# Optimization experiments

Hardware: AMD Instinct MI355X
Metric: run time of the kernel (lower is better)

The kernel has to match this reference:

```python
import jax, jax.numpy as jnp
import numpy as np

H = 16
LN_EPS = 1e-5


def setup_inputs() -> dict:
    key = jax.random.key(0)
    ks = jax.random.split(key, 8)
    B, N, D = 2, 2048, 1024
    s = D ** -0.5
    return {
        "q_s": jax.random.normal(ks[0], (B, N, D), jnp.float32),
        "pos_emb": jax.random.normal(ks[1], (B, N, D), jnp.float32),
        "Wq": jax.random.normal(ks[2], (D, D), jnp.float32) * s,
        "Wk": jax.random.normal(ks[3], (D, D), jnp.float32) * s,
        "Wv": jax.random.normal(ks[4], (D, D), jnp.float32) * s,
        "Wo": jax.random.normal(ks[5], (D, D), jnp.float32) * s,
        "bo": jnp.zeros((D,), jnp.float32),
        "ln_g": jnp.ones((D,), jnp.float32),
        "ln_b": jnp.zeros((D,), jnp.float32),
    }


def _split_heads(t):
    b, n, d = t.shape
    return t.reshape(b, n, H, d // H).transpose(0, 2, 1, 3)  # b h n d


def reference(q_s, pos_emb, Wq, Wk, Wv, Wo, bo, ln_g, ln_b):
    # self-attention: k_s = v_s = q_s
    q = _split_heads(q_s @ Wq)
    k = _split_heads(q_s @ Wk)
    v = _split_heads(q_s @ Wv)
    p = _split_heads(pos_emb)
    scale = q.shape[-1] ** -0.5
    # content-content + content-position attention logits: [b,h,i,j]
    att = (jnp.einsum('bhid,bhjd->bhij', q, k) + jnp.einsum('bhid,bhjd->bhij', q, p)) * scale
    att = jax.nn.softmax(att, axis=-1)
    o = jnp.einsum('bhij,bhjd->bhid', att, v)
    b, h, n, d = o.shape
    o = o.transpose(0, 2, 1, 3).reshape(b, n, h * d)
    o = o @ Wo + bo  # out_layer (dropout rate 0 -> identity)
    x = o + q_s  # residual
    mu = jnp.mean(x, axis=-1, keepdims=True)
    var = jnp.var(x, axis=-1, keepdims=True)
    return (x - mu) * jax.lax.rsqrt(var + LN_EPS) * ln_g + ln_b
```

## Files before the change

### kernel.cpp

```cpp
#include <hip/hip_runtime.h>
#include <hip/hip_bf16.h>
#include <stdint.h>

typedef unsigned short u16;
typedef unsigned int u32;
typedef short s16x8 __attribute__((ext_vector_type(8)));
typedef short s16x4 __attribute__((ext_vector_type(4)));
typedef float f32x4 __attribute__((ext_vector_type(4)));

#define MFMA(a, b, c) __builtin_amdgcn_mfma_f32_16x16x32_bf16((a), (b), (c), 0, 0, 0)

__device__ __forceinline__ u16 f2bf_rte(float f) {
  __hip_bfloat16 h = __float2bfloat16(f);
  u16 u;
  __builtin_memcpy(&u, &h, 2);
  return u;
}

__device__ __forceinline__ void gload16(const u16* g, u16* l) {
  __builtin_amdgcn_global_load_lds((const __attribute__((address_space(1))) u32*)g,
                                   (__attribute__((address_space(3))) u32*)l, 16, 0, 0);
}

__global__ __launch_bounds__(256) void k_cvt(const float* __restrict__ in,
                                             u16* __restrict__ out, int n8) {
  int i = blockIdx.x * 256 + threadIdx.x;
  if (i >= n8) return;
  const f32x4* p = (const f32x4*)(in + (size_t)i * 8);
  f32x4 a = p[0], b = p[1];
  s16x8 o;
  for (int k = 0; k < 4; ++k) o[k] = (short)f2bf_rte(a[k]);
  for (int k = 0; k < 4; ++k) o[4 + k] = (short)f2bf_rte(b[k]);
  *(s16x8*)(out + (size_t)i * 8) = o;
}

__global__ __launch_bounds__(256) void k_transpose_w(const float* __restrict__ W0,
                                                     const float* __restrict__ W1,
                                                     const float* __restrict__ W2,
                                                     const float* __restrict__ W3,
                                                     u16* __restrict__ out) {
  const int z = blockIdx.z;
  const float* in = (z == 0) ? W0 : (z == 1) ? W1 : (z == 2) ? W2 : W3;
  u16* o = out + (size_t)z * 1024 * 1024;
  __shared__ u16 tile[64][65];
  const int t = threadIdx.x, tx = t & 63, ty = t >> 6;
  const int r0 = blockIdx.y * 64, c0 = blockIdx.x * 64;
  for (int rr = 0; rr < 16; ++rr) {
    int row = rr * 4 + ty;
    tile[row][tx] = f2bf_rte(in[(size_t)(r0 + row) * 1024 + c0 + tx]);
  }
  __syncthreads();
  for (int rr = 0; rr < 16; ++rr) {
    int row = rr * 4 + ty;
    o[(size_t)(c0 + row) * 1024 + r0 + tx] = tile[tx][row];
  }
}

__global__ __launch_bounds__(256) void k_transpose_v(const u16* __restrict__ V,
                                                     u16* __restrict__ Vt) {
  __shared__ u16 tile[64][65];
  const int t = threadIdx.x, tx = t & 63, ty = t >> 6;
  const int j0 = blockIdx.x * 64;
  const int bh = blockIdx.y;
  const u16* src = V + (size_t)bh * 2048 * 64;
  u16* dst = Vt + (size_t)bh * 64 * 2048;
  for (int rr = 0; rr < 16; ++rr) {
    int row = rr * 4 + ty;
    tile[row][tx] = src[(size_t)(j0 + row) * 64 + tx];
  }
  __syncthreads();
  for (int rr = 0; rr < 16; ++rr) {
    int d = rr * 4 + ty;
    dst[(size_t)d * 2048 + j0 + tx] = tile[tx][d];
  }
}

__global__ __launch_bounds__(256) void k_qkv_gemm(const u16* __restrict__ X,
                                                  const u16* __restrict__ WT,
                                                  const float* __restrict__ pos,
                                                  u16* __restrict__ Qh,
                                                  u16* __restrict__ Kh,
                                                  u16* __restrict__ Vh) {
  __shared__ u16 As[2][4096];
  __shared__ u16 Bs[2][4096];
  const int t = threadIdx.x;
  const int lane = t & 63, wid = t >> 6;
  const int wr = wid >> 1, wc = wid & 1;
  const int g = lane >> 4, lr = lane & 15;
  const int lin = blockIdx.y * 24 + blockIdx.x;
  const int swz = (lin & 7) * 96 + (lin >> 3);
  const int m0 = (swz / 24) * 128, n0 = (swz % 24) * 128;

  const int srcRow = t >> 2;
  const int srcKsw = ((t & 3) * 8) ^ (((t >> 3) & 3) << 3);
  const u16* aSrc = &X[(size_t)(m0 + srcRow) * 1024 + srcKsw];
  const u16* bSrc = &WT[(size_t)(n0 + srcRow) * 1024 + srcKsw];

  const int csw = (g * 8) ^ (((lr >> 1) & 3) << 3);

  f32x4 acc[4][4] = {};

#define QKV_STAGE(buf, k0)                                   \
  {                                                          \
    gload16(aSrc + (k0), &As[buf][wid * 512]);               \
    gload16(aSrc + 65536 + (k0), &As[buf][wid * 512 + 2048]);\
    gload16(bSrc + (k0), &Bs[buf][wid * 512]);               \
    gload16(bSrc + 65536 + (k0), &Bs[buf][wid * 512 + 2048]);\
  }

  QKV_STAGE(0, 0);
  int cur = 0;
  for (int k0 = 0; k0 < 1024; k0 += 32) {
    __syncthreads();
    if (k0 < 992) QKV_STAGE(cur ^ 1, k0 + 32);
    s16x8 a[4], b[4];
#pragma unroll
    for (int mi = 0; mi < 4; ++mi)
      a[mi] = *(const s16x8*)&As[cur][(wr * 64 + mi * 16 + lr) * 32 + csw];
#pragma unroll
    for (int nj = 0; nj < 4; ++nj)
      b[nj] = *(const s16x8*)&Bs[cur][(wc * 64 + nj * 16 + lr) * 32 + csw];
#pragma unroll
    for (int mi = 0; mi < 4; ++mi)
#pragma unroll
      for (int nj = 0; nj < 4; ++nj)
        acc[mi][nj] = MFMA(a[mi], b[nj], acc[mi][nj]);
    cur ^= 1;
  }
#undef QKV_STAGE

  const float QSCALE = 0.125f * 1.44269504f;
  for (int mi = 0; mi < 4; ++mi) {
    for (int nj = 0; nj < 4; ++nj) {
      const int n_g = n0 + wc * 64 + nj * 16 + lr;
      const int buf = n_g >> 10;
      const int col = n_g & 1023;
      const int h = col >> 6, d = col & 63;
      u16* dst = (buf == 0) ? Qh : ((buf == 1) ? Kh : Vh);
      for (int r = 0; r < 4; ++r) {
        const int row = m0 + wr * 64 + mi * 16 + g * 4 + r;
        const int b = row >> 11, n = row & 2047;
        float v = acc[mi][nj][r];
        if (buf == 1) v += pos[(size_t)row * 1024 + col];
        if (buf == 0) v *= QSCALE;
        dst[(size_t)((b * 16 + h) * 2048 + n) * 64 + d] = f2bf_rte(v);
      }
    }
  }
}

__global__ __launch_bounds__(256, 2) void k_attn(const u16* __restrict__ Qh,
                                                 const u16* __restrict__ Kh,
                                                 const u16* __restrict__ Vt,
                                                 u16* __restrict__ Oh) {
  const int t = threadIdx.x, lane = t & 63, wid = t >> 6;
  const int g = lane >> 4, lr = lane & 15;
  const int hid = blockIdx.x;
  const int lid = (hid & 7) * 64 + (hid >> 3);
  const int bh = lid >> 4, itile = lid & 15;
  const int i0 = itile * 128 + wid * 16;

  __shared__ char Ks[2][8192];
  __shared__ char Vs[2][8192];

  const u16* Qp = Qh + (size_t)bh * 2048 * 64;
  const u16* Kp = Kh + (size_t)bh * 2048 * 64;
  const u16* Vp = Vt + (size_t)bh * 64 * 2048;

  s16x8 aq0[2], aq1[2];
  aq0[0] = *(const s16x8*)&Qp[(size_t)(i0 + lr) * 64 + g * 8];
  aq0[1] = *(const s16x8*)&Qp[(size_t)(i0 + lr) * 64 + 32 + g * 8];
  aq1[0] = *(const s16x8*)&Qp[(size_t)(i0 + 64 + lr) * 64 + g * 8];
  aq1[1] = *(const s16x8*)&Qp[(size_t)(i0 + 64 + lr) * 64 + 32 + g * 8];

  f32x4 oa0[4] = {}, oa1[4] = {};
  float m0s = -1e30f, m1s = -1e30f, l0s = 0.f, l1s = 0.f;

  const int srow = t >> 3;
  const int sch = (t & 7) * 16;
  const int swz = (srow & 7) << 4;
  const int sb0 = (srow * 128 + sch) ^ swz;
  const int sb1 = ((srow + 32) * 128 + sch) ^ swz;
  const u16* kB0 = &Kp[(size_t)srow * 64 + (sch >> 1)];
  const u16* kB1 = &Kp[(size_t)(srow + 32) * 64 + (sch >> 1)];
  const u16* vB0 = &Vp[(size_t)srow * 2048 + (sch >> 1)];
  const u16* vB1 = &Vp[(size_t)(srow + 32) * 2048 + (sch >> 1)];

  s16x8 kr0 = *(const s16x8*)kB0;
  s16x8 kr1 = *(const s16x8*)kB1;
  s16x8 vr0 = *(const s16x8*)vB0;
  s16x8 vr1 = *(const s16x8*)vB1;
  *(s16x8*)(Ks[0] + sb0) = kr0;
  *(s16x8*)(Ks[0] + sb1) = kr1;
  *(s16x8*)(Vs[0] + sb0) = vr0;
  *(s16x8*)(Vs[0] + sb1) = vr1;
  __syncthreads();

  const int src0 = ((g & 1) * 2) * 16 + lr;
  const int src1 = src0 + 16;

  for (int tt = 0; tt < 32; ++tt) {
    const int cur = tt & 1;
    if (tt < 31) {
      const size_t j1 = (size_t)(tt + 1) * 64;
      kr0 = *(const s16x8*)(kB0 + j1 * 64);
      kr1 = *(const s16x8*)(kB1 + j1 * 64);
      vr0 = *(const s16x8*)(vB0 + j1);
      vr1 = *(const s16x8*)(vB1 + j1);
    }
    const char* Kc = Ks[cur];
    const char* Vc = Vs[cur];

    f32x4 s0[4] = {}, s1[4] = {};
    __builtin_amdgcn_s_setprio(1);
#pragma unroll
    for (int jf = 0; jf < 4; ++jf) {
      const int row = jf * 16 + lr;
      const int bw = (row & 7) << 4;
      s16x8 bk0 = *(const s16x8*)(Kc + ((row * 128 + g * 16) ^ bw));
      s16x8 bk1 = *(const s16x8*)(Kc + ((row * 128 + 64 + g * 16) ^ bw));
      s0[jf] = MFMA(bk0, aq0[0], s0[jf]);
      s0[jf] = MFMA(bk1, aq0[1], s0[jf]);
      s1[jf] = MFMA(bk0, aq1[0], s1[jf]);
      s1[jf] = MFMA(bk1, aq1[1], s1[jf]);
    }
    __builtin_amdgcn_s_setprio(0);

    float tl0 = s0[0][0], tl1 = s1[0][0];
#pragma unroll
    for (int jf = 0; jf < 4; ++jf)
#pragma unroll
      for (int r = 0; r < 4; ++r) {
        if (jf | r) {
          tl0 = fmaxf(tl0, s0[jf][r]);
          tl1 = fmaxf(tl1, s1[jf][r]);
        }
      }
    int ok = (tl0 <= m0s + 8.f) & (tl1 <= m1s + 8.f);
    if (!__all(ok)) {
      float tm0 = fmaxf(tl0, __shfl_xor(tl0, 16, 64));
      tm0 = fmaxf(tm0, __shfl_xor(tm0, 32, 64));
      float tm1 = fmaxf(tl1, __shfl_xor(tl1, 16, 64));
      tm1 = fmaxf(tm1, __shfl_xor(tm1, 32, 64));
      float mn0 = fmaxf(m0s, tm0), mn1 = fmaxf(m1s, tm1);
      float al0 = __builtin_amdgcn_exp2f(m0s - mn0);
      float al1 = __builtin_amdgcn_exp2f(m1s - mn1);
      l0s *= al0; m0s = mn0;
      l1s *= al1; m1s = mn1;
#pragma unroll
      for (int r = 0; r < 4; ++r) {
        float ab0 = __shfl(al0, g * 4 + r, 64);
        float ab1 = __shfl(al1, g * 4 + r, 64);
#pragma unroll
        for (int df = 0; df < 4; ++df) {
          oa0[df][r] *= ab0;
          oa1[df][r] *= ab1;
        }
      }
    }

#pragma unroll
    for (int jf = 0; jf < 4; ++jf)
#pragma unroll
      for (int r = 0; r < 4; ++r) {
        float p0 = __builtin_amdgcn_exp2f(s0[jf][r] - m0s);
        float p1 = __builtin_amdgcn_exp2f(s1[jf][r] - m1s);
        s0[jf][r] = p0; l0s += p0;
        s1[jf][r] = p1; l1s += p1;
      }

    u32 pk0[4][2], pk1[4][2];
#pragma unroll
    for (int jf = 0; jf < 4; ++jf) {
      asm("v_cvt_pk_bf16_f32 %0, %1, %2" : "=v"(pk0[jf][0]) : "v"(s0[jf][0]), "v"(s0[jf][1]));
      asm("v_cvt_pk_bf16_f32 %0, %1, %2" : "=v"(pk0[jf][1]) : "v"(s0[jf][2]), "v"(s0[jf][3]));
      asm("v_cvt_pk_bf16_f32 %0, %1, %2" : "=v"(pk1[jf][0]) : "v"(s1[jf][0]), "v"(s1[jf][1]));
      asm("v_cvt_pk_bf16_f32 %0, %1, %2" : "=v"(pk1[jf][1]) : "v"(s1[jf][2]), "v"(s1[jf][3]));
    }

    s16x8 pa0[2], pa1[2];
#pragma unroll
    for (int c = 0; c < 2; ++c) {
      u32 a0 = (u32)__shfl((int)pk0[2 * c][0], src0, 64);
      u32 a1 = (u32)__shfl((int)pk0[2 * c][1], src0, 64);
      u32 a2 = (u32)__shfl((int)pk0[2 * c][0], src1, 64);
      u32 a3 = (u32)__shfl((int)pk0[2 * c][1], src1, 64);
      u32 b0 = (u32)__shfl((int)pk0[2 * c + 1][0], src0, 64);
      u32 b1 = (u32)__shfl((int)pk0[2 * c + 1][1], src0, 64);
      u32 b2 = (u32)__shfl((int)pk0[2 * c + 1][0], src1, 64);
      u32 b3 = (u32)__shfl((int)pk0[2 * c + 1][1], src1, 64);
      u32 w[4];
      w[0] = (g & 2) ? b0 : a0;
      w[1] = (g & 2) ? b1 : a1;
      w[2] = (g & 2) ? b2 : a2;
      w[3] = (g & 2) ? b3 : a3;
      __builtin_memcpy(&pa0[c], w, 16);
      u32 c0 = (u32)__shfl((int)pk1[2 * c][0], src0, 64);
      u32 c1 = (u32)__shfl((int)pk1[2 * c][1], src0, 64);
      u32 c2 = (u32)__shfl((int)pk1[2 * c][0], src1, 64);
      u32 c3 = (u32)__shfl((int)pk1[2 * c][1], src1, 64);
      u32 d0 = (u32)__shfl((int)pk1[2 * c + 1][0], src0, 64);
      u32 d1 = (u32)__shfl((int)pk1[2 * c + 1][1], src0, 64);
      u32 d2 = (u32)__shfl((int)pk1[2 * c + 1][0], src1, 64);
      u32 d3 = (u32)__shfl((int)pk1[2 * c + 1][1], src1, 64);
      u32 x[4];
      x[0] = (g & 2) ? d0 : c0;
      x[1] = (g & 2) ? d1 : c1;
      x[2] = (g & 2) ? d2 : c2;
      x[3] = (g & 2) ? d3 : c3;
      __builtin_memcpy(&pa1[c], x, 16);
    }

    __builtin_amdgcn_s_setprio(1);
#pragma unroll
    for (int df = 0; df < 4; ++df) {
      const int row = df * 16 + lr;
      const int bw = (row & 7) << 4;
      s16x8 bv0 = *(const s16x8*)(Vc + ((row * 128 + g * 16) ^ bw));
      s16x8 bv1 = *(const s16x8*)(Vc + ((row * 128 + 64 + g * 16) ^ bw));
      oa0[df] = MFMA(pa0[0], bv0, oa0[df]);
      oa0[df] = MFMA(pa0[1], bv1, oa0[df]);
      oa1[df] = MFMA(pa1[0], bv0, oa1[df]);
      oa1[df] = MFMA(pa1[1], bv1, oa1[df]);
    }
    __builtin_amdgcn_s_setprio(0);

    if (tt < 31) {
      char* Kn = Ks[cur ^ 1];
      char* Vn = Vs[cur ^ 1];
      *(s16x8*)(Kn + sb0) = kr0;
      *(s16x8*)(Kn + sb1) = kr1;
      *(s16x8*)(Vn + sb0) = vr0;
      *(s16x8*)(Vn + sb1) = vr1;
    }
    __syncthreads();
  }

  l0s += __shfl_xor(l0s, 16, 64);
  l0s += __shfl_xor(l0s, 32, 64);
  l1s += __shfl_xor(l1s, 16, 64);
  l1s += __shfl_xor(l1s, 32, 64);

  float lb0[4], lb1[4];
#pragma unroll
  for (int r = 0; r < 4; ++r) {
    lb0[r] = __shfl(l0s, g * 4 + r, 64);
    lb1[r] = __shfl(l1s, g * 4 + r, 64);
  }

  u16* Op = Oh + (size_t)bh * 2048 * 64;
#pragma unroll
  for (int df = 0; df < 4; ++df)
#pragma unroll
    for (int r = 0; r < 4; ++r) {
      const int row0 = i0 + g * 4 + r;
      Op[(size_t)row0 * 64 + df * 16 + lr] = f2bf_rte(oa0[df][r] / lb0[r]);
      Op[(size_t)(row0 + 64) * 64 + df * 16 + lr] = f2bf_rte(oa1[df][r] / lb1[r]);
    }
}

__global__ __launch_bounds__(256) void k_out_gemm(const u16* __restrict__ Oh,
                                                  const u16* __restrict__ WTo,
                                                  const float* __restrict__ bo,
                                                  const float* __restrict__ qs,
                                                  float* __restrict__ X) {
  __shared__ u16 As[2][4096];
  __shared__ u16 Bs[2][4096];
  const int t = threadIdx.x;
  const int lane = t & 63, wid = t >> 6;
  const int wr = wid >> 1, wc = wid & 1;
  const int g = lane >> 4, lr = lane & 15;
  const int lin = blockIdx.y * 8 + blockIdx.x;
  const int swz = (lin & 7) * 32 + (lin >> 3);
  const int m0 = (swz / 8) * 128, n0 = (swz % 8) * 128;

  const int srcRow = t >> 2;
  const int srcKsw = ((t & 3) * 8) ^ (((t >> 3) & 3) << 3);
  const int rg = m0 + srcRow, bb0 = rg >> 11, nn0 = rg & 2047;
  const int rg2 = rg + 64, bb2 = rg2 >> 11, nn2 = rg2 & 2047;
  const u16* bSrc = &WTo[(size_t)(n0 + srcRow) * 1024 + srcKsw];
  const int csw = (g * 8) ^ (((lr >> 1) & 3) << 3);

  f32x4 acc[4][4] = {};

#define OUT_STAGE(buf, k0)                                                        \
  {                                                                               \
    const int h_ = (k0) >> 6, d_ = ((k0) & 63) + srcKsw;                          \
    gload16(&Oh[((size_t)(bb0 * 16 + h_) * 2048 + nn0) * 64 + d_],                \
            &As[buf][wid * 512]);                                                 \
    gload16(&Oh[((size_t)(bb2 * 16 + h_) * 2048 + nn2) * 64 + d_],                \
            &As[buf][wid * 512 + 2048]);                                          \
    gload16(bSrc + (k0), &Bs[buf][wid * 512]);                                    \
    gload16(bSrc + 65536 + (k0), &Bs[buf][wid * 512 + 2048]);                     \
  }

  OUT_STAGE(0, 0);
  int cur = 0;
  for (int k0 = 0; k0 < 1024; k0 += 32) {
    __syncthreads();
    if (k0 < 992) OUT_STAGE(cur ^ 1, k0 + 32);
    s16x8 a[4], b[4];
#pragma unroll
    for (int mi = 0; mi < 4; ++mi)
      a[mi] = *(const s16x8*)&As[cur][(wr * 64 + mi * 16 + lr) * 32 + csw];
#pragma unroll
    for (int nj = 0; nj < 4; ++nj)
      b[nj] = *(const s16x8*)&Bs[cur][(wc * 64 + nj * 16 + lr) * 32 + csw];
#pragma unroll
    for (int mi = 0; mi < 4; ++mi)
#pragma unroll
      for (int nj = 0; nj < 4; ++nj)
        acc[mi][nj] = MFMA(a[mi], b[nj], acc[mi][nj]);
    cur ^= 1;
  }
#undef OUT_STAGE

  for (int mi = 0; mi < 4; ++mi) {
    for (int nj = 0; nj < 4; ++nj) {
      const int col = n0 + wc * 64 + nj * 16 + lr;
      for (int r = 0; r < 4; ++r) {
        const int row = m0 + wr * 64 + mi * 16 + g * 4 + r;
        float v = acc[mi][nj][r] + bo[col] + qs[(size_t)row * 1024 + col];
        X[(size_t)row * 1024 + col] = v;
      }
    }
  }
}

__global__ __launch_bounds__(256) void k_ln(const float* __restrict__ X,
                                            const float* __restrict__ gg,
                                            const float* __restrict__ bb,
                                            float* __restrict__ out) {
  const int row = blockIdx.x, t = threadIdx.x;
  const int wid = t >> 6, lane = t & 63;
  const float* xr = X + (size_t)row * 1024;
  f32x4 x = *(const f32x4*)&xr[t * 4];
  float s1 = x[0] + x[1] + x[2] + x[3];
  float s2 = x[0] * x[0] + x[1] * x[1] + x[2] * x[2] + x[3] * x[3];
  for (int off = 32; off > 0; off >>= 1) {
    s1 += __shfl_down(s1, off, 64);
    s2 += __shfl_down(s2, off, 64);
  }
  __shared__ float red[2][4];
  if (lane == 0) { red[0][wid] = s1; red[1][wid] = s2; }
  __syncthreads();
  s1 = red[0][0] + red[0][1] + red[0][2] + red[0][3];
  s2 = red[1][0] + red[1][1] + red[1][2] + red[1][3];
  const float mu = s1 * (1.f / 1024.f);
  const float var = s2 * (1.f / 1024.f) - mu * mu;
  const float rstd = rsqrtf(var + 1e-5f);
  f32x4 gv = *(const f32x4*)&gg[t * 4];
  f32x4 bv = *(const f32x4*)&bb[t * 4];
  f32x4 ov;
  for (int i = 0; i < 4; ++i) ov[i] = (x[i] - mu) * rstd * gv[i] + bv[i];
  *(f32x4*)&out[(size_t)row * 1024 + t * 4] = ov;
}

extern "C" void kernel_launch(void* const* d_in, const int* in_sizes, int n_in,
                              void* d_out, int out_size, void* d_ws, size_t ws_size,
                              hipStream_t stream) {
  (void)in_sizes; (void)n_in; (void)out_size; (void)ws_size;
  const float* q_s = (const float*)d_in[0];
  const float* pos = (const float*)d_in[1];
  const float* Wq = (const float*)d_in[2];
  const float* Wk = (const float*)d_in[3];
  const float* Wv = (const float*)d_in[4];
  const float* Wo = (const float*)d_in[5];
  const float* bo = (const float*)d_in[6];
  const float* lng = (const float*)d_in[7];
  const float* lnb = (const float*)d_in[8];
  float* out = (float*)d_out;

  u16* ws = (u16*)d_ws;
  const size_t MB1 = 1024 * 1024;
  u16* WT  = ws;
  u16* Xbf = ws + 4 * MB1;
  u16* Qh  = Xbf + 4 * MB1;
  u16* Kh  = Qh + 4 * MB1;
  u16* Vh  = Kh + 4 * MB1;
  u16* Vt  = Vh + 4 * MB1;
  u16* Oh  = Vt + 4 * MB1;
  float* Xb = (float*)Qh;

  dim3 blk(256);
  k_cvt<<<dim3(2048), blk, 0, stream>>>(q_s, Xbf, 4 * MB1 / 8);
  k_transpose_w<<<dim3(16, 16, 4), blk, 0, stream>>>(Wq, Wk, Wv, Wo, WT);
  k_qkv_gemm<<<dim3(24, 32), blk, 0, stream>>>(Xbf, WT, pos, Qh, Kh, Vh);
  k_transpose_v<<<dim3(32, 32), blk, 0, stream>>>(Vh, Vt);
  k_attn<<<dim3(512), blk, 0, stream>>>(Qh, Kh, Vt, Oh);
  k_out_gemm<<<dim3(8, 32), blk, 0, stream>>>(Oh, WT + 3 * MB1, bo, q_s, Xb);
  k_ln<<<4096, blk, 0, stream>>>(Xb, lng, lnb, out);
}
```

Baseline: 155.4 us.

## Split attention work across 8 waves with 16 query rows each

Doubles the attention block to 512 threads so each wave processes one 16-row query tile instead of two, while the block still covers 128 query rows. K/V tile staging is spread across all 512 threads with one 16-byte load each. This lowers per-wave register use and raises resident waves for latency hiding. In exchange, each K/V fragment read from LDS is reused for only one query tile, doubling LDS reads per MFMA, and block-wide barriers now cover more waves.

```diff
diff --git a/kernel.cpp b/kernel.cpp
--- a/kernel.cpp
+++ b/kernel.cpp
@@ -149,7 +149,7 @@
   }
 }
 
-__global__ __launch_bounds__(256, 2) void k_attn(const u16* __restrict__ Qh,
+__global__ __launch_bounds__(512, 4) void k_attn(const u16* __restrict__ Qh,
                                                  const u16* __restrict__ Kh,
                                                  const u16* __restrict__ Vt,
                                                  u16* __restrict__ Oh) {
@@ -167,33 +167,24 @@
   const u16* Kp = Kh + (size_t)bh * 2048 * 64;
   const u16* Vp = Vt + (size_t)bh * 64 * 2048;
 
-  s16x8 aq0[2], aq1[2];
-  aq0[0] = *(const s16x8*)&Qp[(size_t)(i0 + lr) * 64 + g * 8];
-  aq0[1] = *(const s16x8*)&Qp[(size_t)(i0 + lr) * 64 + 32 + g * 8];
-  aq1[0] = *(const s16x8*)&Qp[(size_t)(i0 + 64 + lr) * 64 + g * 8];
-  aq1[1] = *(const s16x8*)&Qp[(size_t)(i0 + 64 + lr) * 64 + 32 + g * 8];
-
-  f32x4 oa0[4] = {}, oa1[4] = {};
-  float m0s = -1e30f, m1s = -1e30f, l0s = 0.f, l1s = 0.f;
+  s16x8 aq[2];
+  aq[0] = *(const s16x8*)&Qp[(size_t)(i0 + lr) * 64 + g * 8];
+  aq[1] = *(const s16x8*)&Qp[(size_t)(i0 + lr) * 64 + 32 + g * 8];
+
+  f32x4 oa[4] = {};
+  float ms = -1e30f, ls = 0.f;
 
   const int srow = t >> 3;
   const int sch = (t & 7) * 16;
   const int swz = (srow & 7) << 4;
-  const int sb0 = (srow * 128 + sch) ^ swz;
-  const int sb1 = ((srow + 32) * 128 + sch) ^ swz;
-  const u16* kB0 = &Kp[(size_t)srow * 64 + (sch >> 1)];
-  const u16* kB1 = &Kp[(size_t)(srow + 32) * 64 + (sch >> 1)];
-  const u16* vB0 = &Vp[(size_t)srow * 2048 + (sch >> 1)];
-  const u16* vB1 = &Vp[(size_t)(srow + 32) * 2048 + (sch >> 1)];
-
-  s16x8 kr0 = *(const s16x8*)kB0;
-  s16x8 kr1 = *(const s16x8*)kB1;
-  s16x8 vr0 = *(const s16x8*)vB0;
-  s16x8 vr1 = *(const s16x8*)vB1;
-  *(s16x8*)(Ks[0] + sb0) = kr0;
-  *(s16x8*)(Ks[0] + sb1) = kr1;
-  *(s16x8*)(Vs[0] + sb0) = vr0;
-  *(s16x8*)(Vs[0] + sb1) = vr1;
+  const int sb = (srow * 128 + sch) ^ swz;
+  const u16* kB = &Kp[(size_t)srow * 64 + (sch >> 1)];
+  const u16* vB = &Vp[(size_t)srow * 2048 + (sch >> 1)];
+
+  s16x8 kr = *(const s16x8*)kB;
+  s16x8 vr = *(const s16x8*)vB;
+  *(s16x8*)(Ks[0] + sb) = kr;
+  *(s16x8*)(Vs[0] + sb) = vr;
   __syncthreads();
 
   const int src0 = ((g & 1) * 2) * 16 + lr;
@@ -203,15 +194,13 @@
     const int cur = tt & 1;
     if (tt < 31) {
       const size_t j1 = (size_t)(tt + 1) * 64;
-      kr0 = *(const s16x8*)(kB0 + j1 * 64);
-      kr1 = *(const s16x8*)(kB1 + j1 * 64);
-      vr0 = *(const s16x8*)(vB0 + j1);
-      vr1 = *(const s16x8*)(vB1 + j1);
+      kr = *(const s16x8*)(kB + j1 * 64);
+      vr = *(const s16x8*)(vB + j1);
     }
     const char* Kc = Ks[cur];
     const char* Vc = Vs[cur];
 
-    f32x4 s0[4] = {}, s1[4] = {};
+    f32x4 s[4] = {};
     __builtin_amdgcn_s_setprio(1);
 #pragma unroll
     for (int jf = 0; jf < 4; ++jf) {
@@ -219,96 +208,65 @@
       const int bw = (row & 7) << 4;
       s16x8 bk0 = *(const s16x8*)(Kc + ((row * 128 + g * 16) ^ bw));
       s16x8 bk1 = *(const s16x8*)(Kc + ((row * 128 + 64 + g * 16) ^ bw));
-      s0[jf] = MFMA(bk0, aq0[0], s0[jf]);
-      s0[jf] = MFMA(bk1, aq0[1], s0[jf]);
-      s1[jf] = MFMA(bk0, aq1[0], s1[jf]);
-      s1[jf] = MFMA(bk1, aq1[1], s1[jf]);
+      s[jf] = MFMA(bk0, aq[0], s[jf]);
+      s[jf] = MFMA(bk1, aq[1], s[jf]);
     }
     __builtin_amdgcn_s_setprio(0);
 
-    float tl0 = s0[0][0], tl1 = s1[0][0];
+    float tl = s[0][0];
 #pragma unroll
     for (int jf = 0; jf < 4; ++jf)
 #pragma unroll
+      for (int r = 0; r < 4; ++r)
+        if (jf | r) tl = fmaxf(tl, s[jf][r]);
+    if (!__all(tl <= ms + 8.f)) {
+      float tm = fmaxf(tl, __shfl_xor(tl, 16, 64));
+      tm = fmaxf(tm, __shfl_xor(tm, 32, 64));
+      float mn = fmaxf(ms, tm);
+      float al = __builtin_amdgcn_exp2f(ms - mn);
+      ls *= al;
+      ms = mn;
+#pragma unroll
       for (int r = 0; r < 4; ++r) {
-        if (jf | r) {
-          tl0 = fmaxf(tl0, s0[jf][r]);
-          tl1 = fmaxf(tl1, s1[jf][r]);
-        }
+        float ab = __shfl(al, g * 4 + r, 64);
+#pragma unroll
+        for (int df = 0; df < 4; ++df) oa[df][r] *= ab;
       }
-    int ok = (tl0 <= m0s + 8.f) & (tl1 <= m1s + 8.f);
-    if (!__all(ok)) {
-      float tm0 = fmaxf(tl0, __shfl_xor(tl0, 16, 64));
-      tm0 = fmaxf(tm0, __shfl_xor(tm0, 32, 64));
-      float tm1 = fmaxf(tl1, __shfl_xor(tl1, 16, 64));
-      tm1 = fmaxf(tm1, __shfl_xor(tm1, 32, 64));
-      float mn0 = fmaxf(m0s, tm0), mn1 = fmaxf(m1s, tm1);
-      float al0 = __builtin_amdgcn_exp2f(m0s - mn0);
-      float al1 = __builtin_amdgcn_exp2f(m1s - mn1);
-      l0s *= al0; m0s = mn0;
-      l1s *= al1; m1s = mn1;
+    }
+
+#pragma unroll
+    for (int jf = 0; jf < 4; ++jf)
 #pragma unroll
       for (int r = 0; r < 4; ++r) {
-        float ab0 = __shfl(al0, g * 4 + r, 64);
-        float ab1 = __shfl(al1, g * 4 + r, 64);
-#pragma unroll
-        for (int df = 0; df < 4; ++df) {
-          oa0[df][r] *= ab0;
-          oa1[df][r] *= ab1;
-        }
+        float p = __builtin_amdgcn_exp2f(s[jf][r] - ms);
+        s[jf][r] = p;
+        ls += p;
       }
-    }
-
-#pragma unroll
-    for (int jf = 0; jf < 4; ++jf)
-#pragma unroll
-      for (int r = 0; r < 4; ++r) {
-        float p0 = __builtin_amdgcn_exp2f(s0[jf][r] - m0s);
-        float p1 = __builtin_amdgcn_exp2f(s1[jf][r] - m1s);
-        s0[jf][r] = p0; l0s += p0;
-        s1[jf][r] = p1; l1s += p1;
-      }
-
-    u32 pk0[4][2], pk1[4][2];
+
+    u32 pk[4][2];
 #pragma unroll
     for (int jf = 0; jf < 4; ++jf) {
-      asm("v_cvt_pk_bf16_f32 %0, %1, %2" : "=v"(pk0[jf][0]) : "v"(s0[jf][0]), "v"(s0[jf][1]));
-      asm("v_cvt_pk_bf16_f32 %0, %1, %2" : "=v"(pk0[jf][1]) : "v"(s0[jf][2]), "v"(s0[jf][3]));
-      asm("v_cvt_pk_bf16_f32 %0, %1, %2" : "=v"(pk1[jf][0]) : "v"(s1[jf][0]), "v"(s1[jf][1]));
-      asm("v_cvt_pk_bf16_f32 %0, %1, %2" : "=v"(pk1[jf][1]) : "v"(s1[jf][2]), "v"(s1[jf][3]));
-    }
-
-    s16x8 pa0[2], pa1[2];
+      asm("v_cvt_pk_bf16_f32 %0, %1, %2" : "=v"(pk[jf][0]) : "v"(s[jf][0]), "v"(s[jf][1]));
+      asm("v_cvt_pk_bf16_f32 %0, %1, %2" : "=v"(pk[jf][1]) : "v"(s[jf][2]), "v"(s[jf][3]));
+    }
+
+    s16x8 pa[2];
 #pragma unroll
     for (int c = 0; c < 2; ++c) {
-      u32 a0 = (u32)__shfl((int)pk0[2 * c][0], src0, 64);
-      u32 a1 = (u32)__shfl((int)pk0[2 * c][1], src0, 64);
-      u32 a2 = (u32)__shfl((int)pk0[2 * c][0], src1, 64);
-      u32 a3 = (u32)__shfl((int)pk0[2 * c][1], src1, 64);
-      u32 b0 = (u32)__shfl((int)pk0[2 * c + 1][0], src0, 64);
-      u32 b1 = (u32)__shfl((int)pk0[2 * c + 1][1], src0, 64);
-      u32 b2 = (u32)__shfl((int)pk0[2 * c + 1][0], src1, 64);
-      u32 b3 = (u32)__shfl((int)pk0[2 * c + 1][1], src1, 64);
+      u32 a0 = (u32)__shfl((int)pk[2 * c][0], src0, 64);
+      u32 a1 = (u32)__shfl((int)pk[2 * c][1], src0, 64);
+      u32 a2 = (u32)__shfl((int)pk[2 * c][0], src1, 64);
+      u32 a3 = (u32)__shfl((int)pk[2 * c][1], src1, 64);
+      u32 b0 = (u32)__shfl((int)pk[2 * c + 1][0], src0, 64);
+      u32 b1 = (u32)__shfl((int)pk[2 * c + 1][1], src0, 64);
+      u32 b2 = (u32)__shfl((int)pk[2 * c + 1][0], src1, 64);
+      u32 b3 = (u32)__shfl((int)pk[2 * c + 1][1], src1, 64);
       u32 w[4];
       w[0] = (g & 2) ? b0 : a0;
       w[1] = (g & 2) ? b1 : a1;
       w[2] = (g & 2) ? b2 : a2;
       w[3] = (g & 2) ? b3 : a3;
-      __builtin_memcpy(&pa0[c], w, 16);
-      u32 c0 = (u32)__shfl((int)pk1[2 * c][0], src0, 64);
-      u32 c1 = (u32)__shfl((int)pk1[2 * c][1], src0, 64);
-      u32 c2 = (u32)__shfl((int)pk1[2 * c][0], src1, 64);
-      u32 c3 = (u32)__shfl((int)pk1[2 * c][1], src1, 64);
-      u32 d0 = (u32)__shfl((int)pk1[2 * c + 1][0], src0, 64);
-      u32 d1 = (u32)__shfl((int)pk1[2 * c + 1][1], src0, 64);
-      u32 d2 = (u32)__shfl((int)pk1[2 * c + 1][0], src1, 64);
-      u32 d3 = (u32)__shfl((int)pk1[2 * c + 1][1], src1, 64);
-      u32 x[4];
-      x[0] = (g & 2) ? d0 : c0;
-      x[1] = (g & 2) ? d1 : c1;
-      x[2] = (g & 2) ? d2 : c2;
-      x[3] = (g & 2) ? d3 : c3;
-      __builtin_memcpy(&pa1[c], x, 16);
+      __builtin_memcpy(&pa[c], w, 16);
     }
 
     __builtin_amdgcn_s_setprio(1);
@@ -318,35 +276,23 @@
       const int bw = (row & 7) << 4;
       s16x8 bv0 = *(const s16x8*)(Vc + ((row * 128 + g * 16) ^ bw));
       s16x8 bv1 = *(const s16x8*)(Vc + ((row * 128 + 64 + g * 16) ^ bw));
-      oa0[df] = MFMA(pa0[0], bv0, oa0[df]);
-      oa0[df] = MFMA(pa0[1], bv1, oa0[df]);
-      oa1[df] = MFMA(pa1[0], bv0, oa1[df]);
-      oa1[df] = MFMA(pa1[1], bv1, oa1[df]);
+      oa[df] = MFMA(pa[0], bv0, oa[df]);
+      oa[df] = MFMA(pa[1], bv1, oa[df]);
     }
     __builtin_amdgcn_s_setprio(0);
 
     if (tt < 31) {
-      char* Kn = Ks[cur ^ 1];
-      char* Vn = Vs[cur ^ 1];
-      *(s16x8*)(Kn + sb0) = kr0;
-      *(s16x8*)(Kn + sb1) = kr1;
-      *(s16x8*)(Vn + sb0) = vr0;
-      *(s16x8*)(Vn + sb1) = vr1;
+      *(s16x8*)(Ks[cur ^ 1] + sb) = kr;
+      *(s16x8*)(Vs[cur ^ 1] + sb) = vr;
     }
     __syncthreads();
   }
 
-  l0s += __shfl_xor(l0s, 16, 64);
-  l0s += __shfl_xor(l0s, 32, 64);
-  l1s += __shfl_xor(l1s, 16, 64);
-  l1s += __shfl_xor(l1s, 32, 64);
-
-  float lb0[4], lb1[4];
-#pragma unroll
-  for (int r = 0; r < 4; ++r) {
-    lb0[r] = __shfl(l0s, g * 4 + r, 64);
-    lb1[r] = __shfl(l1s, g * 4 + r, 64);
-  }
+  ls += __shfl_xor(ls, 16, 64);
+  ls += __shfl_xor(ls, 32, 64);
+  float lb[4];
+#pragma unroll
+  for (int r = 0; r < 4; ++r) lb[r] = __shfl(ls, g * 4 + r, 64);
 
   u16* Op = Oh + (size_t)bh * 2048 * 64;
 #pragma unroll
@@ -354,8 +300,7 @@
 #pragma unroll
     for (int r = 0; r < 4; ++r) {
       const int row0 = i0 + g * 4 + r;
-      Op[(size_t)row0 * 64 + df * 16 + lr] = f2bf_rte(oa0[df][r] / lb0[r]);
-      Op[(size_t)(row0 + 64) * 64 + df * 16 + lr] = f2bf_rte(oa1[df][r] / lb1[r]);
+      Op[(size_t)row0 * 64 + df * 16 + lr] = f2bf_rte(oa[df][r] / lb[r]);
     }
 }
 
@@ -487,7 +432,7 @@
   k_transpose_w<<<dim3(16, 16, 4), blk, 0, stream>>>(Wq, Wk, Wv, Wo, WT);
   k_qkv_gemm<<<dim3(24, 32), blk, 0, stream>>>(Xbf, WT, pos, Qh, Kh, Vh);
   k_transpose_v<<<dim3(32, 32), blk, 0, stream>>>(Vh, Vt);
-  k_attn<<<dim3(512), blk, 0, stream>>>(Qh, Kh, Vt, Oh);
+  k_attn<<<dim3(512), dim3(512), 0, stream>>>(Qh, Kh, Vt, Oh);
   k_out_gemm<<<dim3(8, 32), blk, 0, stream>>>(Oh, WT + 3 * MB1, bo, q_s, Xb);
   k_ln<<<4096, blk, 0, stream>>>(Xb, lng, lnb, out);
 }
```

New measurement: 158.0 us. No clear change (+1.7%).
